# Optimization experiments

Hardware: AMD Instinct MI355X
Metric: run time of the kernel (lower is better)

The kernel has to match this reference:

```python
import jax, jax.numpy as jnp
import numpy as np

Q_MAX = 127.0  # int8 activation quant range
NIB_MASK = 15  # 4-bit mask


def setup_inputs() -> dict:
    key = jax.random.key(0)
    k1, k2, k3, k4, k5 = jax.random.split(key, 5)
    M, IN, OUT = 4096, 4096, 11008
    x = jax.random.normal(k1, (M, IN), dtype=jnp.float32)
    # packed int4 weights: two nibbles per byte, [OUT, IN//2]
    qweight = jax.random.randint(k2, (OUT, IN // 2), 0, 256, dtype=jnp.int32)
    qzeros = jax.random.randint(k3, (OUT, 1), 0, 16, dtype=jnp.int32)
    scales = jax.random.uniform(k4, (OUT, 1), dtype=jnp.float32) * 0.01 + 1e-4
    bias = jax.random.normal(k5, (OUT,), dtype=jnp.float32) * 0.01
    clampv = jnp.full((1,), 3.0, dtype=jnp.float32)
    return {"x": x, "qweight": qweight, "qzeros": qzeros,
            "scales": scales, "bias": bias, "clampv": clampv}


def _unpack_int4(qweight, qzeros, scales):
    # high nibble -> even position, low nibble -> odd position (matches torch unpack)
    hi = (qweight >> 4) & NIB_MASK          # [OUT, IN//2]
    lo = qweight & NIB_MASK                 # [OUT, IN//2]
    intw = jnp.stack([hi, lo], axis=-1).reshape(qweight.shape[0], -1)  # [OUT, IN]
    return (intw - qzeros).astype(scales.dtype) * scales               # [OUT, IN]


def reference(x, qweight, qzeros, scales, bias, clampv):
    cv = clampv[0]
    # static activation fake-quant at scale clampv/127 (quantize_activation_static)
    x = jnp.clip(x, -cv, cv)
    a_scale = cv / Q_MAX
    qx = jnp.clip(jnp.round(x / a_scale), -Q_MAX, Q_MAX) * a_scale
    # dequantize packed int4 weights, then GEMM
    W = _unpack_int4(qweight, qzeros, scales)   # [OUT, IN]
    out = qx @ W.T + bias[None, :]              # [M, OUT]
    return out
```

## Files before the change

### kernel.cpp

```cpp
#include <hip/hip_runtime.h>
#include <stdint.h>

typedef int v4i  __attribute__((ext_vector_type(4)));
typedef int v16i __attribute__((ext_vector_type(16)));

static constexpr int Mdim = 4096;
static constexpr int Kdim = 4096;
static constexpr int Ndim = 11008;

#define BM 256
#define BN 256
#define BK 128
#define NT (Kdim / BK)

__device__ __forceinline__ void gload_lds16(const void* gp, void* lp) {
  __builtin_amdgcn_global_load_lds((const __attribute__((address_space(1))) void*)gp,
                                   (__attribute__((address_space(3))) void*)lp,
                                   16, 0, 0);
}

__global__ void k_quant(const float* __restrict__ x, const float* __restrict__ clampv,
                        signed char* __restrict__ qa, int* __restrict__ rowsum) {
  const int row = blockIdx.x;
  const int t = threadIdx.x;
  const float cv = clampv[0];
  const float a_scale = cv / 127.0f;
  const float4* xp = (const float4*)(x + (size_t)row * Kdim) + t * 4;
  int s = 0;
  int w[4];
#pragma unroll
  for (int i = 0; i < 4; ++i) {
    float4 f = xp[i];
    float q0 = fminf(fmaxf(rintf(fminf(fmaxf(f.x, -cv), cv) / a_scale), -127.f), 127.f);
    float q1 = fminf(fmaxf(rintf(fminf(fmaxf(f.y, -cv), cv) / a_scale), -127.f), 127.f);
    float q2 = fminf(fmaxf(rintf(fminf(fmaxf(f.z, -cv), cv) / a_scale), -127.f), 127.f);
    float q3 = fminf(fmaxf(rintf(fminf(fmaxf(f.w, -cv), cv) / a_scale), -127.f), 127.f);
    int i0 = (int)q0, i1 = (int)q1, i2 = (int)q2, i3 = (int)q3;
    s += i0 + i1 + i2 + i3;
    w[i] = (i0 & 255) | ((i1 & 255) << 8) | ((i2 & 255) << 16) | ((i3 & 255) << 24);
  }
  ((int4*)(qa + (size_t)row * Kdim))[t] = make_int4(w[0], w[1], w[2], w[3]);
#pragma unroll
  for (int off = 32; off > 0; off >>= 1) s += __shfl_down(s, off, 64);
  __shared__ int red[4];
  if ((t & 63) == 0) red[t >> 6] = s;
  __syncthreads();
  if (t == 0) rowsum[row] = red[0] + red[1] + red[2] + red[3];
}

__global__ void k_unpack(const int4* __restrict__ qw, uint2* __restrict__ wb) {
  const int idx = blockIdx.x * 256 + threadIdx.x;
  int4 q = qw[idx];
  uint2 r;
  r.x = (unsigned)(((q.x >> 4) & 15) | ((q.x & 15) << 8) |
                   (((q.y >> 4) & 15) << 16) | ((q.y & 15) << 24));
  r.y = (unsigned)(((q.z >> 4) & 15) | ((q.z & 15) << 8) |
                   (((q.w >> 4) & 15) << 16) | ((q.w & 15) << 24));
  wb[idx] = r;
}

__global__ __launch_bounds__(512, 2) void k_gemm(
    const signed char* __restrict__ A, const signed char* __restrict__ B,
    const float* __restrict__ scales, const int* __restrict__ qzeros,
    const float* __restrict__ bias, const float* __restrict__ clampv,
    const int* __restrict__ rowsum, float* __restrict__ out) {
  __shared__ signed char lds[131072];
  signed char* As = lds;
  signed char* Bs = lds + 65536;

  const int t = threadIdx.x;
  const int lane = t & 63;
  const int wave = t >> 6;
  const int wm = (wave >> 2) * 128;
  const int wn = (wave & 3) * 64;

  const int bid = blockIdx.x;
  const int swz = (bid & 7) * 86 + (bid >> 3);
  const int mt = swz / 43;
  const int nt = swz - mt * 43;
  const int m0 = mt * BM;
  const int n0 = nt * BN;

  const int srow = t >> 3;
  const int sch = (t & 7) ^ (srow & 7);
  const signed char* gA = A + (size_t)(m0 + srow) * Kdim + sch * 16;
  const signed char* gB = B + (size_t)(n0 + srow) * Kdim + sch * 16;
  const int sdst = t * 16;

#define STAGE_A(buf, k0)                                               \
  {                                                                    \
    _Pragma("unroll") for (int i = 0; i < 4; ++i)                      \
        gload_lds16(gA + (size_t)(i * 64) * Kdim + (k0),               \
                    As + (buf) * 32768 + i * 8192 + sdst);             \
  }
#define STAGE_B(buf, k0)                                               \
  {                                                                    \
    _Pragma("unroll") for (int i = 0; i < 4; ++i)                      \
        gload_lds16(gB + (size_t)(i * 64) * Kdim + (k0),               \
                    Bs + (buf) * 32768 + i * 8192 + sdst);             \
  }

  const int col32 = lane & 31;
  const int q32 = lane >> 5;
  const int c7 = lane & 7;
  const int abase = (wm + col32) * BK;
  const int bbase = (wn + col32) * BK;
  int pos[4];
#pragma unroll
  for (int ks = 0; ks < 4; ++ks) pos[ks] = ((ks * 2 + q32) ^ c7) * 16;

  v16i acc[4][2] = {};
  v4i a[2][4], b[2][2];

#define LOADK(bank, ks_)                                                   \
  {                                                                        \
    _Pragma("unroll") for (int i = 0; i < 4; ++i)                          \
        a[bank][i] = *(const v4i*)(Ac + i * 4096 + abase + pos[ks_]);      \
    _Pragma("unroll") for (int j = 0; j < 2; ++j)                          \
        b[bank][j] = *(const v4i*)(Bc + j * 4096 + bbase + pos[ks_]);      \
  }

  STAGE_A(0, 0);
  STAGE_B(0, 0);
  asm volatile("s_waitcnt vmcnt(0)" ::: "memory");
  __builtin_amdgcn_s_barrier();

  int cur = 0;
  for (int ti = 0; ti < NT; ++ti) {
    const int nk = (ti + 1) * BK;
    const bool pf = (ti + 1 < NT);
    const signed char* Ac = As + cur * 32768;
    const signed char* Bc = Bs + cur * 32768;

    if (pf) {
      STAGE_A(cur ^ 1, nk);
      STAGE_B(cur ^ 1, nk);
    }

    LOADK(0, 0);
#pragma unroll
    for (int ks = 0; ks < 4; ++ks) {
      if (ks < 3) LOADK((ks + 1) & 1, ks + 1);
      __builtin_amdgcn_s_setprio(1);
#pragma unroll
      for (int i = 0; i < 4; ++i)
#pragma unroll
        for (int j = 0; j < 2; ++j)
          acc[i][j] = __builtin_amdgcn_mfma_i32_32x32x32_i8(a[ks & 1][i], b[ks & 1][j],
                                                            acc[i][j], 0, 0, 0);
      __builtin_amdgcn_s_setprio(0);
    }

    asm volatile("s_waitcnt vmcnt(0)" ::: "memory");
    __builtin_amdgcn_s_barrier();
    cur ^= 1;
  }
#undef STAGE_A
#undef STAGE_B
#undef LOADK

  const float a_scale = clampv[0] / 127.0f;
#pragma unroll
  for (int j = 0; j < 2; ++j) {
    const int n = n0 + wn + j * 32 + col32;
    const float sn = scales[n] * a_scale;
    const int zn = qzeros[n];
    const float bn = bias[n];
#pragma unroll
    for (int i = 0; i < 4; ++i) {
      const int mbase = m0 + wm + i * 32;
#pragma unroll
      for (int r = 0; r < 16; ++r) {
        const int row = (r & 3) + 8 * (r >> 2) + 4 * q32;
        const int m = mbase + row;
        const int iv = acc[i][j][r] - zn * rowsum[m];
        out[(size_t)m * Ndim + n] = (float)iv * sn + bn;
      }
    }
  }
}

extern "C" void kernel_launch(void* const* d_in, const int* in_sizes, int n_in,
                              void* d_out, int out_size, void* d_ws, size_t ws_size,
                              hipStream_t stream) {
  const float* x  = (const float*)d_in[0];
  const int* qw   = (const int*)d_in[1];
  const int* qz   = (const int*)d_in[2];
  const float* sc = (const float*)d_in[3];
  const float* bi = (const float*)d_in[4];
  const float* cv = (const float*)d_in[5];
  float* out = (float*)d_out;

  signed char* qa = (signed char*)d_ws;
  signed char* wb = qa + (size_t)Mdim * Kdim;
  int* rowsum = (int*)(wb + (size_t)Ndim * Kdim);

  k_quant<<<Mdim, 256, 0, stream>>>(x, cv, qa, rowsum);
  k_unpack<<<(Ndim * (Kdim / 2) / 4) / 256, 256, 0, stream>>>((const int4*)qw, (uint2*)wb);
  k_gemm<<<dim3((Mdim / BM) * (Ndim / BN)), 512, 0, stream>>>(qa, wb, sc, qz, bi, cv, rowsum, out);
}
```

Before: 475.5 us.

## Switch GEMM to 16x16x64 int8 MFMA with K-tile split into two steps

Replaces the 32x32x32 int8 MFMA with the 16x16x64 variant, so each wave computes an 8x4 grid of 16x16 tiles and each 128-wide K tile takes two MFMA steps instead of four. The LDS fragment indexing is reworked for the new operand layout. The last K iteration is peeled out of the loop to drop the prefetch branch. The epilogue preloads rowsum values into registers and writes 16-column fragments. Register pressure grows with twice as many A and B fragments and 32 accumulator vectors, and the output stores now cover only 16 contiguous floats per row instead of 32.

```diff
diff --git a/kernel.cpp b/kernel.cpp
--- a/kernel.cpp
+++ b/kernel.cpp
@@ -1,8 +1,7 @@
 #include <hip/hip_runtime.h>
 #include <stdint.h>
 
-typedef int v4i  __attribute__((ext_vector_type(4)));
-typedef int v16i __attribute__((ext_vector_type(16)));
+typedef int v4i __attribute__((ext_vector_type(4)));
 
 static constexpr int Mdim = 4096;
 static constexpr int Kdim = 4096;
@@ -100,24 +99,35 @@
                     Bs + (buf) * 32768 + i * 8192 + sdst);             \
   }
 
-  const int col32 = lane & 31;
-  const int q32 = lane >> 5;
-  const int c7 = lane & 7;
-  const int abase = (wm + col32) * BK;
-  const int bbase = (wn + col32) * BK;
-  int pos[4];
-#pragma unroll
-  for (int ks = 0; ks < 4; ++ks) pos[ks] = ((ks * 2 + q32) ^ c7) * 16;
-
-  v16i acc[4][2] = {};
-  v4i a[2][4], b[2][2];
-
-#define LOADK(bank, ks_)                                                   \
-  {                                                                        \
-    _Pragma("unroll") for (int i = 0; i < 4; ++i)                          \
-        a[bank][i] = *(const v4i*)(Ac + i * 4096 + abase + pos[ks_]);      \
-    _Pragma("unroll") for (int j = 0; j < 2; ++j)                          \
-        b[bank][j] = *(const v4i*)(Bc + j * 4096 + bbase + pos[ks_]);      \
+  const int col = lane & 15;
+  const int q16 = lane >> 4;
+  const int c7 = col & 7;
+  int aoff[2], boff[2];
+#pragma unroll
+  for (int ks = 0; ks < 2; ++ks) {
+    const int pos = ((ks * 4 + q16) ^ c7) * 16;
+    aoff[ks] = (wm + col) * BK + pos;
+    boff[ks] = (wn + col) * BK + pos;
+  }
+
+  v4i acc[8][4] = {};
+  v4i a[2][8], b[2][4];
+
+#define LOADK(bank, ks_)                                                    \
+  {                                                                         \
+    _Pragma("unroll") for (int i = 0; i < 8; ++i)                           \
+        a[bank][i] = *(const v4i*)(Ac + i * 2048 + aoff[ks_]);              \
+    _Pragma("unroll") for (int j = 0; j < 4; ++j)                           \
+        b[bank][j] = *(const v4i*)(Bc + j * 2048 + boff[ks_]);              \
+  }
+#define MFMAK(bank)                                                         \
+  {                                                                         \
+    __builtin_amdgcn_s_setprio(1);                                          \
+    _Pragma("unroll") for (int i = 0; i < 8; ++i)                           \
+        _Pragma("unroll") for (int j = 0; j < 4; ++j)                       \
+            acc[i][j] = __builtin_amdgcn_mfma_i32_16x16x64_i8(              \
+                a[bank][i], b[bank][j], acc[i][j], 0, 0, 0);                \
+    __builtin_amdgcn_s_setprio(0);                                          \
   }
 
   STAGE_A(0, 0);
@@ -126,55 +136,57 @@
   __builtin_amdgcn_s_barrier();
 
   int cur = 0;
-  for (int ti = 0; ti < NT; ++ti) {
+  for (int ti = 0; ti < NT - 1; ++ti) {
     const int nk = (ti + 1) * BK;
-    const bool pf = (ti + 1 < NT);
     const signed char* Ac = As + cur * 32768;
     const signed char* Bc = Bs + cur * 32768;
 
-    if (pf) {
-      STAGE_A(cur ^ 1, nk);
-      STAGE_B(cur ^ 1, nk);
-    }
+    STAGE_A(cur ^ 1, nk);
+    STAGE_B(cur ^ 1, nk);
 
     LOADK(0, 0);
-#pragma unroll
-    for (int ks = 0; ks < 4; ++ks) {
-      if (ks < 3) LOADK((ks + 1) & 1, ks + 1);
-      __builtin_amdgcn_s_setprio(1);
-#pragma unroll
-      for (int i = 0; i < 4; ++i)
-#pragma unroll
-        for (int j = 0; j < 2; ++j)
-          acc[i][j] = __builtin_amdgcn_mfma_i32_32x32x32_i8(a[ks & 1][i], b[ks & 1][j],
-                                                            acc[i][j], 0, 0, 0);
-      __builtin_amdgcn_s_setprio(0);
-    }
+    LOADK(1, 1);
+    MFMAK(0);
+    MFMAK(1);
 
     asm volatile("s_waitcnt vmcnt(0)" ::: "memory");
     __builtin_amdgcn_s_barrier();
     cur ^= 1;
   }
+  {
+    const signed char* Ac = As + cur * 32768;
+    const signed char* Bc = Bs + cur * 32768;
+    LOADK(0, 0);
+    LOADK(1, 1);
+    MFMAK(0);
+    MFMAK(1);
+  }
 #undef STAGE_A
 #undef STAGE_B
 #undef LOADK
+#undef MFMAK
 
   const float a_scale = clampv[0] / 127.0f;
-#pragma unroll
-  for (int j = 0; j < 2; ++j) {
-    const int n = n0 + wn + j * 32 + col32;
+  const int rq = q16 * 4;
+  int rs[8][4];
+#pragma unroll
+  for (int i = 0; i < 8; ++i)
+#pragma unroll
+    for (int r = 0; r < 4; ++r)
+      rs[i][r] = rowsum[m0 + wm + i * 16 + rq + r];
+#pragma unroll
+  for (int j = 0; j < 4; ++j) {
+    const int n = n0 + wn + j * 16 + col;
     const float sn = scales[n] * a_scale;
     const int zn = qzeros[n];
     const float bn = bias[n];
 #pragma unroll
-    for (int i = 0; i < 4; ++i) {
-      const int mbase = m0 + wm + i * 32;
-#pragma unroll
-      for (int r = 0; r < 16; ++r) {
-        const int row = (r & 3) + 8 * (r >> 2) + 4 * q32;
-        const int m = mbase + row;
-        const int iv = acc[i][j][r] - zn * rowsum[m];
-        out[(size_t)m * Ndim + n] = (float)iv * sn + bn;
+    for (int i = 0; i < 8; ++i) {
+      const int mb = m0 + wm + i * 16 + rq;
+#pragma unroll
+      for (int r = 0; r < 4; ++r) {
+        const int iv = acc[i][j][r] - zn * rs[i][r];
+        out[(size_t)(mb + r) * Ndim + n] = (float)iv * sn + bn;
       }
     }
   }
```

New measurement: 462.4 us. 2.8% less time.
